# Optimization experiments

Hardware: AMD Instinct MI355X
Metric: run time of the kernel (lower is better)

## Reference

```python
import jax, jax.numpy as jnp
import numpy as np

NUM_HEADS = 16
ROPE_BASE = 10000.0


def _rope_cos_sin(seq_len, head_dim, dtype):
    inv_freq = 1.0 / (ROPE_BASE ** (jnp.arange(0, head_dim, 2, dtype=jnp.float32) / head_dim))
    t = jnp.arange(seq_len, dtype=jnp.float32)
    freqs = t[:, None] * inv_freq[None, :]          # [S, hd/2]
    emb = jnp.concatenate([freqs, freqs], axis=-1)  # [S, hd]
    return jnp.cos(emb).astype(dtype), jnp.sin(emb).astype(dtype)


def _rotate_half(x):
    x1, x2 = jnp.split(x, 2, axis=-1)
    return jnp.concatenate([-x2, x1], axis=-1)


def setup_inputs() -> dict:
    key = jax.random.key(0)
    ks = jax.random.split(key, 5)
    B, S, D = 2, 2048, 2048
    x = jax.random.normal(ks[0], (B, S, D), dtype=jnp.float32)
    Wq = jax.random.normal(ks[1], (D, D), dtype=jnp.float32) * (D ** -0.5)
    Wk = jax.random.normal(ks[2], (D, D), dtype=jnp.float32) * (D ** -0.5)
    Wv = jax.random.normal(ks[3], (D, D), dtype=jnp.float32) * (D ** -0.5)
    Wo = jax.random.normal(ks[4], (D, D), dtype=jnp.float32) * (D ** -0.5)
    return {"x": x, "Wq": Wq, "Wk": Wk, "Wv": Wv, "Wo": Wo}


def reference(x, Wq, Wk, Wv, Wo):
    B, S, D = x.shape
    H = NUM_HEADS
    hd = D // H
    scale = hd ** -0.5
    # Linear(bias=False): y = x @ W.T ; reshape to [B, H, S, hd]
    def proj(W):
        return jnp.einsum('bsd,ed->bse', x, W).reshape(B, S, H, hd).transpose(0, 2, 1, 3)
    q, k, v = proj(Wq), proj(Wk), proj(Wv)
    cos, sin = _rope_cos_sin(S, hd, x.dtype)  # [S, hd]
    cos = cos[None, None, :, :]
    sin = sin[None, None, :, :]
    q = q * cos + _rotate_half(q) * sin
    k = k * cos + _rotate_half(k) * sin
    scores = jnp.einsum('bhqd,bhkd->bhqk', q, k) * scale  # [B,H,S,S]
    causal = jnp.triu(jnp.ones((S, S), dtype=bool), k=1)
    scores = jnp.where(causal[None, None], jnp.finfo(scores.dtype).min, scores)
    attn = jax.nn.softmax(scores, axis=-1)
    out = jnp.einsum('bhqk,bhkd->bhqd', attn, v)  # [B,H,S,hd]
    out = out.transpose(0, 2, 1, 3).reshape(B, S, D)
    return jnp.einsum('bsd,ed->bse', out, Wo)
```

## Files before the change

kernel.cpp:

```cpp
#include <hip/hip_runtime.h>
#include <hip/hip_bf16.h>
#include <math.h>

typedef __bf16 bf16_t;
typedef __attribute__((ext_vector_type(8))) __bf16 bf16x8;
typedef __attribute__((ext_vector_type(4))) float f32x4;
typedef __attribute__((ext_vector_type(16))) float f32x16;

#define S_LEN 2048
#define DM    2048
#define NH    16
#define HD    128
#define MTOT  4096

__device__ inline float finz(float v) {
    return (v == v && fabsf(v) < 1e30f) ? v : 0.f;
}

__device__ inline void gload_lds16(const bf16_t* g, bf16_t* l) {
    __builtin_amdgcn_global_load_lds(
        (const __attribute__((address_space(1))) void*)g,
        (__attribute__((address_space(3))) void*)l, 16, 0, 0);
}

__device__ __forceinline__ int crow4(int g, int hi) {
    return (g & 3) + ((g >> 2) << 3) + (hi << 2);
}
__device__ __forceinline__ unsigned pk2(float x, float y) {
    union { bf16_t h; unsigned short u; } a, b;
    a.h = (bf16_t)x; b.h = (bf16_t)y;
    return (unsigned)a.u | ((unsigned)b.u << 16);
}
__device__ __forceinline__ bf16x8 pack4(unsigned w0, unsigned w1, unsigned w2, unsigned w3) {
    union { unsigned w[4]; bf16x8 v; } u;
    u.w[0] = w0; u.w[1] = w1; u.w[2] = w2; u.w[3] = w3;
    return u.v;
}

#define MFMA16(a, b, c) __builtin_amdgcn_mfma_f32_16x16x32_bf16(a, b, c, 0, 0, 0)
#define MFMA32(a, b, c) __builtin_amdgcn_mfma_f32_32x32x16_bf16(a, b, c, 0, 0, 0)

__global__ __launch_bounds__(256)
void dtype_probe(const unsigned short* __restrict__ p, unsigned int* __restrict__ flag)
{
    __shared__ int tot;
    if (threadIdx.x == 0) tot = 0;
    __syncthreads();
    int weird = 0;
    for (int i = threadIdx.x; i < 4096; i += 256) {
        unsigned short u = p[2*i];
        int e = (u >> 7) & 0xFF;
        if (e >= 0xC8 || (e != 0 && e <= 0x38)) weird++;
    }
    atomicAdd(&tot, weird);
    __syncthreads();
    if (threadIdx.x == 0) *flag = (tot > 512) ? 1u : 0u;
}

__global__ __launch_bounds__(256)
void convert_all(const void* __restrict__ x_raw,
                 const void* __restrict__ w0, const void* __restrict__ w1,
                 const void* __restrict__ w2, const void* __restrict__ w3,
                 bf16_t* __restrict__ xb, bf16_t* __restrict__ wb,
                 float2* __restrict__ rtab,
                 int mode, const unsigned int* __restrict__ flag)
{
    const int bid = blockIdx.x;
    if (bid >= 25088) return;
    if (bid >= 24576) {
        int i = (bid - 24576)*256 + threadIdx.x;
        int s = i >> 6, t64 = i & 63;
        float invf = exp2f(-(float)t64 * 0.20762050593046014f);
        float ang  = (float)s * invf;
        float sn, cs;
        sincosf(ang, &sn, &cs);
        rtab[i] = make_float2(cs, sn);
        return;
    }
    const bool f32 = (mode == 2) ? (*flag != 0) : (mode == 1);
    const void* src; bf16_t* dst; int i;
    if (bid < 8192) {
        src = x_raw; dst = xb; i = bid*1024 + threadIdx.x*4;
    } else {
        int w  = (bid - 8192) >> 12;
        int lb = (bid - 8192) & 4095;
        src = (w == 0) ? w0 : (w == 1) ? w1 : (w == 2) ? w2 : w3;
        dst = wb + (size_t)w * DM * DM;
        i = lb*1024 + threadIdx.x*4;
    }
    if (f32) {
        const float4 v = *(const float4*)((const float*)src + i);
        dst[i  ] = (bf16_t)v.x; dst[i+1] = (bf16_t)v.y;
        dst[i+2] = (bf16_t)v.z; dst[i+3] = (bf16_t)v.w;
    } else {
        *(uint2*)(dst + i) = *(const uint2*)((const bf16_t*)src + i);
    }
}

template<int MODE>
__global__ __launch_bounds__(256)
void gemm_bt(const bf16_t* __restrict__ A, const bf16_t* __restrict__ W,
             void* __restrict__ Cv, const float2* __restrict__ rtab)
{
    __shared__ __align__(16) bf16_t Sh[2*128*64];
    bf16_t* As = Sh;
    bf16_t* Ws = Sh + 128*64;

    const int t    = threadIdx.x;
    const int wv   = t >> 6;
    const int lane = t & 63;
    const int c16  = lane & 15;
    const int quad = lane >> 4;
    const int wm   = wv & 1;
    const int wn   = wv >> 1;
    const int mb   = blockIdx.x;
    const int nb   = blockIdx.y;
    const int c7   = c16 & 7;

    const int srow = lane >> 3;
    const int sphy = (lane & 7) ^ srow;
    const bf16_t* Ab = A + (size_t)(mb*128 + wv*32 + srow)*DM + sphy*8;
    const bf16_t* Wb = W + (size_t)(nb*128 + wv*32 + srow)*DM + sphy*8;

    f32x4 acc[4][4];
    #pragma unroll
    for (int i = 0; i < 4; ++i)
        #pragma unroll
        for (int j = 0; j < 4; ++j)
            acc[i][j] = (f32x4){0.f, 0.f, 0.f, 0.f};

    for (int kb = 0; kb < DM/64; ++kb) {
        __syncthreads();
        #pragma unroll
        for (int i = 0; i < 4; ++i) {
            gload_lds16(Ab + (size_t)kb*64 + (size_t)i*8*DM, As + (wv*32 + i*8)*64);
            gload_lds16(Wb + (size_t)kb*64 + (size_t)i*8*DM, Ws + (wv*32 + i*8)*64);
        }
        __syncthreads();

        #pragma unroll
        for (int kk = 0; kk < 2; ++kk) {
            const int ph = ((kk*4 + quad) ^ c7) * 8;
            bf16x8 af[4], bfr[4];
            #pragma unroll
            for (int mt = 0; mt < 4; ++mt)
                af[mt] = *(const bf16x8*)(As + (wm*64 + mt*16 + c16)*64 + ph);
            #pragma unroll
            for (int nt = 0; nt < 4; ++nt)
                bfr[nt] = *(const bf16x8*)(Ws + (nt*32 + wn*16 + c16)*64 + ph);
            #pragma unroll
            for (int mt = 0; mt < 4; ++mt)
                #pragma unroll
                for (int nt = 0; nt < 4; ++nt)
                    acc[mt][nt] = MFMA16(af[mt], bfr[nt], acc[mt][nt]);
        }
    }

    if (MODE == 4 && nb >= 32) {
        __syncthreads();
        #pragma unroll
        for (int mt = 0; mt < 4; ++mt) {
            #pragma unroll
            for (int r = 0; r < 4; ++r) {
                const int sl = wm*64 + mt*16 + quad*4 + r;
                #pragma unroll
                for (int nt = 0; nt < 4; ++nt) {
                    const int dl = nt*32 + wn*16 + c16;
                    Sh[dl*128 + (sl ^ ((dl & 15) << 3))] =
                        (bf16_t)finz(acc[mt][nt][r]);
                }
            }
        }
        __syncthreads();
        const int hh  = nb & 15;
        const int b   = (mb*128) >> 11;
        const int s0t = (mb*128) & (S_LEN - 1);
        bf16_t* VT = (bf16_t*)Cv + (size_t)2 * MTOT * DM;
        #pragma unroll
        for (int p = 0; p < 8; ++p) {
            int idx = p*256 + t;
            int dl  = idx >> 4;
            int s0  = (idx & 15) * 8;
            bf16x8 v = *(const bf16x8*)&Sh[dl*128 + (s0 ^ ((dl & 15) << 3))];
            *(bf16x8*)((bf16_t*)VT +
                ((size_t)(b*NH + hh)*HD + dl)*S_LEN + s0t + s0) = v;
        }
        return;
    }

    #pragma unroll
    for (int mt = 0; mt < 4; ++mt) {
        #pragma unroll
        for (int r = 0; r < 4; ++r) {
            const int m = mb*128 + wm*64 + mt*16 + quad*4 + r;
            if (MODE == 2) {
                bf16_t* C = (bf16_t*)Cv;
                size_t base = (size_t)m*DM + nb*128;
                #pragma unroll
                for (int nt = 0; nt < 4; ++nt)
                    C[base + nt*32 + wn*16 + c16] = (bf16_t)finz(acc[mt][nt][r]);
            } else if (MODE == 3) {
                float* C = (float*)Cv;
                size_t base = (size_t)m*DM + nb*128;
                #pragma unroll
                for (int nt = 0; nt < 4; ++nt)
                    C[base + nt*32 + wn*16 + c16] = finz(acc[mt][nt][r]);
            } else {
                const int g  = nb >> 4;
                const int hh = nb & 15;
                bf16_t* C = (bf16_t*)Cv + (size_t)g * MTOT * DM;
                const int b = m >> 11;
                const int s = m & (S_LEN - 1);
                size_t base = ((size_t)(b*NH + hh)*S_LEN + s)*HD;
                #pragma unroll
                for (int nt = 0; nt < 2; ++nt) {
                    int t64 = nt*32 + wn*16 + c16;
                    float2 cs2 = rtab[s*64 + t64];
                    float lo  = acc[mt][nt  ][r];
                    float hi2 = acc[mt][nt+2][r];
                    C[base + t64     ] = (bf16_t)finz(lo*cs2.x - hi2*cs2.y);
                    C[base + t64 + 64] = (bf16_t)finz(hi2*cs2.x + lo*cs2.y);
                }
            }
        }
    }
}

__global__ __launch_bounds__(512, 2)
void flash_attn(const bf16_t* __restrict__ Q, const bf16_t* __restrict__ K,
                const bf16_t* __restrict__ VT, bf16_t* __restrict__ O)
{
    __shared__ bf16_t Ks[64*128];
    __shared__ bf16_t Vs[128*64];
    __shared__ float  Ocmb[4][32*128];
    __shared__ float  lcmb[4][32];

    const int t    = threadIdx.x;
    const int wid  = t >> 6;
    const int lane = t & 63;
    const int qw   = wid & 3;
    const int kh   = wid >> 2;
    const int c32  = lane & 31;
    const int hi   = lane >> 5;
    const int bh   = blockIdx.x;
    const int ix   = blockIdx.y;

    const float scale = 0.08838834764831845f;
    const float SMAX  = 12.0f;

    bf16x8 onesf;
    #pragma unroll
    for (int j = 0; j < 8; ++j) onesf[j] = (bf16_t)1.0f;

    for (int pass = 0; pass < 2; ++pass) {
        const int Qt   = pass ? (15 - ix) : ix;
        const int qt0  = Qt * 128;
        const int qrow = qt0 + qw*32 + c32;
        const int qmin = qt0 + qw*32;

        bf16x8 qf[8];
        {
            const bf16_t* qp = Q + ((size_t)bh*S_LEN + qrow)*HD;
            #pragma unroll
            for (int s = 0; s < 8; ++s)
                qf[s] = *(const bf16x8*)(qp + s*16 + hi*8);
        }

        f32x16 oacc[4];
        f32x16 lacc;
        #pragma unroll
        for (int e = 0; e < 16; ++e) lacc[e] = 0.f;
        #pragma unroll
        for (int dt = 0; dt < 4; ++dt)
            #pragma unroll
            for (int e = 0; e < 16; ++e) oacc[dt][e] = 0.f;

        const int ktend = 2*Qt + 1;
        for (int kt = 0; kt <= ktend; ++kt) {
            __syncthreads();
            #pragma unroll
            for (int j = 0; j < 2; ++j) {
                int base = wid*8 + j*4;
                int rg   = base + (lane >> 4);
                int ph   = (lane & 15) ^ (rg & 7);
                gload_lds16(K + ((size_t)bh*S_LEN + kt*64 + rg)*HD + ph*8,
                            Ks + base*128);
            }
            #pragma unroll
            for (int j = 0; j < 2; ++j) {
                int base = wid*16 + j*8;
                int rg   = base + (lane >> 3);
                int ph   = (lane & 7) ^ (rg & 7);
                gload_lds16(VT + ((size_t)bh*HD + rg)*S_LEN + kt*64 + ph*8,
                            Vs + base*64);
            }
            __syncthreads();

            const int kbase = kt*64 + kh*32;
            if (kbase > qmin + 31) continue;

            f32x16 sacc;
            #pragma unroll
            for (int e = 0; e < 16; ++e) sacc[e] = 0.f;
            const int krow = kh*32 + c32;
            const int ksw  = krow & 7;
            __builtin_amdgcn_s_setprio(1);
            #pragma unroll
            for (int s = 0; s < 8; ++s) {
                bf16x8 kf = *(const bf16x8*)(Ks + krow*128 + (((s*2 + hi) ^ ksw) << 3));
                sacc = MFMA32(kf, qf[s], sacc);
            }
            __builtin_amdgcn_s_setprio(0);

            float p[16];
            if (kbase + 31 > qmin) {
                #pragma unroll
                for (int g = 0; g < 16; ++g) {
                    int kg = kbase + crow4(g, hi);
                    p[g] = (kg <= qrow) ? __expf(sacc[g]*scale - SMAX) : 0.f;
                }
            } else {
                #pragma unroll
                for (int g = 0; g < 16; ++g)
                    p[g] = __expf(sacc[g]*scale - SMAX);
            }

            unsigned a0 = pk2(p[0],  p[1]),  b0 = pk2(p[2],  p[3]);
            unsigned a1 = pk2(p[4],  p[5]),  b1 = pk2(p[6],  p[7]);
            unsigned a2 = pk2(p[8],  p[9]),  b2 = pk2(p[10], p[11]);
            unsigned a3 = pk2(p[12], p[13]), b3 = pk2(p[14], p[15]);
            asm volatile("v_permlane32_swap_b32 %0, %1" : "+v"(a0), "+v"(a1));
            asm volatile("v_permlane32_swap_b32 %0, %1" : "+v"(b0), "+v"(b1));
            asm volatile("v_permlane32_swap_b32 %0, %1" : "+v"(a2), "+v"(a3));
            asm volatile("v_permlane32_swap_b32 %0, %1" : "+v"(b2), "+v"(b3));
            bf16x8 pa0 = pack4(a0, b0, a1, b1);
            bf16x8 pa1 = pack4(a2, b2, a3, b3);

            const int ks0 = kh*2 + 0, ks1 = kh*2 + 1;
            __builtin_amdgcn_s_setprio(1);
            lacc = MFMA32(pa0, onesf, lacc);
            lacc = MFMA32(pa1, onesf, lacc);
            #pragma unroll
            for (int dt = 0; dt < 4; ++dt) {
                const int vrow = dt*32 + c32;
                const int vsw  = vrow & 7;
                bf16x8 vf0 = *(const bf16x8*)(Vs + vrow*64 + (((ks0*2 + hi) ^ vsw) << 3));
                oacc[dt] = MFMA32(pa0, vf0, oacc[dt]);
                bf16x8 vf1 = *(const bf16x8*)(Vs + vrow*64 + (((ks1*2 + hi) ^ vsw) << 3));
                oacc[dt] = MFMA32(pa1, vf1, oacc[dt]);
            }
            __builtin_amdgcn_s_setprio(0);
        }

        if (kh == 1) {
            #pragma unroll
            for (int g = 0; g < 16; ++g) {
                int ql = crow4(g, hi);
                #pragma unroll
                for (int dt = 0; dt < 4; ++dt)
                    Ocmb[qw][ql*128 + dt*32 + c32] = oacc[dt][g];
            }
            if (c32 == 0) {
                #pragma unroll
                for (int g = 0; g < 16; ++g)
                    lcmb[qw][crow4(g, hi)] = lacc[g];
            }
        }
        __syncthreads();
        if (kh == 0) {
            const int b = bh >> 4, h = bh & 15;
            #pragma unroll
            for (int g = 0; g < 16; ++g) {
                int ql = crow4(g, hi);
                int qg = qt0 + qw*32 + ql;
                float lt = lacc[g] + lcmb[qw][ql];
                float rl = 1.0f / fmaxf(lt, 1e-37f);
                #pragma unroll
                for (int dt = 0; dt < 4; ++dt) {
                    float v = oacc[dt][g] + Ocmb[qw][ql*128 + dt*32 + c32];
                    O[((size_t)(b*S_LEN + qg))*DM + h*HD + dt*32 + c32] =
                        (bf16_t)finz(v*rl);
                }
            }
        }
    }
}

extern "C" void kernel_launch(void* const* d_in, const int* in_sizes, int n_in,
                              void* d_out, int out_size, void* d_ws, size_t ws_size,
                              hipStream_t stream)
{
    const void* x_raw  = d_in[0];
    const void* Wq_raw = d_in[1];
    const void* Wk_raw = d_in[2];
    const void* Wv_raw = d_in[3];
    const void* Wo_raw = d_in[4];

    const int NX = MTOT*DM;
    const int NW = DM*DM;

    unsigned int* flag = (unsigned int*)d_ws;
    bf16_t* xb  = (bf16_t*)((char*)d_ws + 16);
    bf16_t* Wqb = xb  + NX;
    bf16_t* Wkb = Wqb + NW;
    bf16_t* Wvb = Wkb + NW;
    bf16_t* Wob = Wvb + NW;
    bf16_t* Qb  = Wob + NW;
    bf16_t* Kb  = Qb + NX;
    bf16_t* VTb = Kb + NX;
    bf16_t* Ob  = VTb + NX;
    float2* rtab = (float2*)(Ob + NX);

    bool out_is_f32 = true;
    {
        void* base = nullptr; size_t sz = 0;
        if (hipMemGetAddressRange((hipDeviceptr_t*)&base, &sz,
                                  (hipDeviceptr_t)d_out) == hipSuccess && sz != 0) {
            if (sz < (size_t)out_size * 3) out_is_f32 = false;
        }
    }

    int mode = 2;
    if (in_sizes && n_in >= 1) {
        if (in_sizes[0] == NX*4)      mode = 1;
        else if (in_sizes[0] == NX*2) mode = 0;
    }

    dim3 bb(256);
    if (mode == 2)
        hipLaunchKernelGGL(dtype_probe, dim3(1), bb, 0, stream,
                           (const unsigned short*)x_raw, flag);

    hipLaunchKernelGGL(convert_all, dim3(25088), bb, 0, stream,
                       x_raw, Wq_raw, Wk_raw, Wv_raw, Wo_raw,
                       xb, Wqb, rtab, mode, flag);

    hipLaunchKernelGGL((gemm_bt<4>), dim3(32, 48), bb, 0, stream, xb, Wqb,
                       (void*)Qb, rtab);
    hipLaunchKernelGGL(flash_attn, dim3(32, 8), dim3(512), 0, stream, Qb, Kb, VTb, Ob);
    if (out_is_f32)
        hipLaunchKernelGGL((gemm_bt<3>), dim3(32, 16), bb, 0, stream, Ob, Wob,
                           d_out, rtab);
    else
        hipLaunchKernelGGL((gemm_bt<2>), dim3(32, 16), bb, 0, stream, Ob, Wob,
                           d_out, rtab);
}
```

Before: 397.5 us.

## Fuse all stages into one persistent cooperative kernel with grid syncs

Replaces the five separate launches (dtype probe, conversion, QKV GEMM, flash attention, output GEMM) with one cooperative kernel of 256 blocks of 512 threads, separated by grid-wide barriers. Each block runs two 256-thread GEMM tile instances in its shared memory and grid-strides the conversion work. This is meant to remove launch overhead and inter-kernel gaps. In exchange the GEMM phases drop to one 512-thread block per CU with a fixed tile assignment, attention occupancy drops from launch_bounds(512,2) to (512,1), and grid.sync adds its own cost.

```diff
diff --git a/kernel.cpp b/kernel.cpp
--- a/kernel.cpp
+++ b/kernel.cpp
@@ -1,6 +1,9 @@
 #include <hip/hip_runtime.h>
+#include <hip/hip_cooperative_groups.h>
 #include <hip/hip_bf16.h>
 #include <math.h>
+
+namespace cg = cooperative_groups;
 
 typedef __bf16 bf16_t;
 typedef __attribute__((ext_vector_type(8))) __bf16 bf16x8;
@@ -40,81 +43,20 @@
 #define MFMA16(a, b, c) __builtin_amdgcn_mfma_f32_16x16x32_bf16(a, b, c, 0, 0, 0)
 #define MFMA32(a, b, c) __builtin_amdgcn_mfma_f32_32x32x16_bf16(a, b, c, 0, 0, 0)
 
-__global__ __launch_bounds__(256)
-void dtype_probe(const unsigned short* __restrict__ p, unsigned int* __restrict__ flag)
+__device__ __forceinline__ void gemm_tile(
+    bf16_t* __restrict__ Shm, const bf16_t* __restrict__ A,
+    const bf16_t* __restrict__ W, void* __restrict__ Cv,
+    const float2* __restrict__ rtab, int mb, int nb, int mode, int t)
 {
-    __shared__ int tot;
-    if (threadIdx.x == 0) tot = 0;
-    __syncthreads();
-    int weird = 0;
-    for (int i = threadIdx.x; i < 4096; i += 256) {
-        unsigned short u = p[2*i];
-        int e = (u >> 7) & 0xFF;
-        if (e >= 0xC8 || (e != 0 && e <= 0x38)) weird++;
-    }
-    atomicAdd(&tot, weird);
-    __syncthreads();
-    if (threadIdx.x == 0) *flag = (tot > 512) ? 1u : 0u;
-}
-
-__global__ __launch_bounds__(256)
-void convert_all(const void* __restrict__ x_raw,
-                 const void* __restrict__ w0, const void* __restrict__ w1,
-                 const void* __restrict__ w2, const void* __restrict__ w3,
-                 bf16_t* __restrict__ xb, bf16_t* __restrict__ wb,
-                 float2* __restrict__ rtab,
-                 int mode, const unsigned int* __restrict__ flag)
-{
-    const int bid = blockIdx.x;
-    if (bid >= 25088) return;
-    if (bid >= 24576) {
-        int i = (bid - 24576)*256 + threadIdx.x;
-        int s = i >> 6, t64 = i & 63;
-        float invf = exp2f(-(float)t64 * 0.20762050593046014f);
-        float ang  = (float)s * invf;
-        float sn, cs;
-        sincosf(ang, &sn, &cs);
-        rtab[i] = make_float2(cs, sn);
-        return;
-    }
-    const bool f32 = (mode == 2) ? (*flag != 0) : (mode == 1);
-    const void* src; bf16_t* dst; int i;
-    if (bid < 8192) {
-        src = x_raw; dst = xb; i = bid*1024 + threadIdx.x*4;
-    } else {
-        int w  = (bid - 8192) >> 12;
-        int lb = (bid - 8192) & 4095;
-        src = (w == 0) ? w0 : (w == 1) ? w1 : (w == 2) ? w2 : w3;
-        dst = wb + (size_t)w * DM * DM;
-        i = lb*1024 + threadIdx.x*4;
-    }
-    if (f32) {
-        const float4 v = *(const float4*)((const float*)src + i);
-        dst[i  ] = (bf16_t)v.x; dst[i+1] = (bf16_t)v.y;
-        dst[i+2] = (bf16_t)v.z; dst[i+3] = (bf16_t)v.w;
-    } else {
-        *(uint2*)(dst + i) = *(const uint2*)((const bf16_t*)src + i);
-    }
-}
-
-template<int MODE>
-__global__ __launch_bounds__(256)
-void gemm_bt(const bf16_t* __restrict__ A, const bf16_t* __restrict__ W,
-             void* __restrict__ Cv, const float2* __restrict__ rtab)
-{
-    __shared__ __align__(16) bf16_t Sh[2*128*64];
-    bf16_t* As = Sh;
-    bf16_t* Ws = Sh + 128*64;
-
-    const int t    = threadIdx.x;
+    bf16_t* As = Shm;
+    bf16_t* Ws = Shm + 128*64;
+
     const int wv   = t >> 6;
     const int lane = t & 63;
     const int c16  = lane & 15;
     const int quad = lane >> 4;
     const int wm   = wv & 1;
     const int wn   = wv >> 1;
-    const int mb   = blockIdx.x;
-    const int nb   = blockIdx.y;
     const int c7   = c16 & 7;
 
     const int srow = lane >> 3;
@@ -156,8 +98,9 @@
         }
     }
 
-    if (MODE == 4 && nb >= 32) {
-        __syncthreads();
+    const bool vpath = (mode == 4 && nb >= 32);
+    __syncthreads();
+    if (vpath) {
         #pragma unroll
         for (int mt = 0; mt < 4; ++mt) {
             #pragma unroll
@@ -166,12 +109,14 @@
                 #pragma unroll
                 for (int nt = 0; nt < 4; ++nt) {
                     const int dl = nt*32 + wn*16 + c16;
-                    Sh[dl*128 + (sl ^ ((dl & 15) << 3))] =
+                    Shm[dl*128 + (sl ^ ((dl & 15) << 3))] =
                         (bf16_t)finz(acc[mt][nt][r]);
                 }
             }
         }
-        __syncthreads();
+    }
+    __syncthreads();
+    if (vpath) {
         const int hh  = nb & 15;
         const int b   = (mb*128) >> 11;
         const int s0t = (mb*128) & (S_LEN - 1);
@@ -181,9 +126,8 @@
             int idx = p*256 + t;
             int dl  = idx >> 4;
             int s0  = (idx & 15) * 8;
-            bf16x8 v = *(const bf16x8*)&Sh[dl*128 + (s0 ^ ((dl & 15) << 3))];
-            *(bf16x8*)((bf16_t*)VT +
-                ((size_t)(b*NH + hh)*HD + dl)*S_LEN + s0t + s0) = v;
+            bf16x8 v = *(const bf16x8*)&Shm[dl*128 + (s0 ^ ((dl & 15) << 3))];
+            *(bf16x8*)(VT + ((size_t)(b*NH + hh)*HD + dl)*S_LEN + s0t + s0) = v;
         }
         return;
     }
@@ -193,13 +137,13 @@
         #pragma unroll
         for (int r = 0; r < 4; ++r) {
             const int m = mb*128 + wm*64 + mt*16 + quad*4 + r;
-            if (MODE == 2) {
+            if (mode == 2) {
                 bf16_t* C = (bf16_t*)Cv;
                 size_t base = (size_t)m*DM + nb*128;
                 #pragma unroll
                 for (int nt = 0; nt < 4; ++nt)
                     C[base + nt*32 + wn*16 + c16] = (bf16_t)finz(acc[mt][nt][r]);
-            } else if (MODE == 3) {
+            } else if (mode == 3) {
                 float* C = (float*)Cv;
                 size_t base = (size_t)m*DM + nb*128;
                 #pragma unroll
@@ -226,163 +170,276 @@
     }
 }
 
-__global__ __launch_bounds__(512, 2)
-void flash_attn(const bf16_t* __restrict__ Q, const bf16_t* __restrict__ K,
-                const bf16_t* __restrict__ VT, bf16_t* __restrict__ O)
+__global__ __launch_bounds__(512, 1)
+void mha_fused(const void* __restrict__ x_raw,
+               const void* __restrict__ w0, const void* __restrict__ w1,
+               const void* __restrict__ w2, const void* __restrict__ w3,
+               bf16_t* __restrict__ xb, bf16_t* __restrict__ wb,
+               bf16_t* __restrict__ Qb, bf16_t* __restrict__ Ob,
+               void* __restrict__ Cout, float2* __restrict__ rtab,
+               int mode, int outf)
 {
-    __shared__ bf16_t Ks[64*128];
-    __shared__ bf16_t Vs[128*64];
-    __shared__ float  Ocmb[4][32*128];
-    __shared__ float  lcmb[4][32];
-
-    const int t    = threadIdx.x;
-    const int wid  = t >> 6;
-    const int lane = t & 63;
-    const int qw   = wid & 3;
-    const int kh   = wid >> 2;
-    const int c32  = lane & 31;
-    const int hi   = lane >> 5;
-    const int bh   = blockIdx.x;
-    const int ix   = blockIdx.y;
-
-    const float scale = 0.08838834764831845f;
-    const float SMAX  = 12.0f;
-
-    bf16x8 onesf;
-    #pragma unroll
-    for (int j = 0; j < 8; ++j) onesf[j] = (bf16_t)1.0f;
-
-    for (int pass = 0; pass < 2; ++pass) {
-        const int Qt   = pass ? (15 - ix) : ix;
-        const int qt0  = Qt * 128;
-        const int qrow = qt0 + qw*32 + c32;
-        const int qmin = qt0 + qw*32;
-
-        bf16x8 qf[8];
+    __shared__ __align__(16) unsigned char ShRaw[98816];
+    cg::grid_group grid = cg::this_grid();
+
+    const int bid = blockIdx.x;
+    const int t   = threadIdx.x;
+    const int NXE = MTOT*DM;
+    const int NWE = DM*DM;
+
+    {
+        bool f32in;
+        if (mode == 2) {
+            int* tot = (int*)ShRaw;
+            if (t == 0) *tot = 0;
+            __syncthreads();
+            int weird = 0;
+            const unsigned short* p = (const unsigned short*)x_raw;
+            for (int i = t; i < 4096; i += 512) {
+                unsigned short u = p[2*i];
+                int e = (u >> 7) & 0xFF;
+                if (e >= 0xC8 || (e != 0 && e <= 0x38)) weird++;
+            }
+            atomicAdd(tot, weird);
+            __syncthreads();
+            f32in = (*tot > 512);
+            __syncthreads();
+        } else {
+            f32in = (mode == 1);
+        }
+
+        const int gtid = bid*512 + t;
+        const int GSTR = 256*512;
+        if (f32in) {
+            for (int i = gtid; i < NXE/4; i += GSTR) {
+                float4 v = ((const float4*)x_raw)[i];
+                union { bf16_t h[4]; uint2 u; } o;
+                o.h[0] = (bf16_t)v.x; o.h[1] = (bf16_t)v.y;
+                o.h[2] = (bf16_t)v.z; o.h[3] = (bf16_t)v.w;
+                ((uint2*)xb)[i] = o.u;
+            }
+            const void* wsrc[4] = {w0, w1, w2, w3};
+            #pragma unroll
+            for (int w = 0; w < 4; ++w) {
+                const float4* ws = (const float4*)wsrc[w];
+                uint2* wd = (uint2*)(wb + (size_t)w*NWE);
+                for (int i = gtid; i < NWE/4; i += GSTR) {
+                    float4 v = ws[i];
+                    union { bf16_t h[4]; uint2 u; } o;
+                    o.h[0] = (bf16_t)v.x; o.h[1] = (bf16_t)v.y;
+                    o.h[2] = (bf16_t)v.z; o.h[3] = (bf16_t)v.w;
+                    wd[i] = o.u;
+                }
+            }
+        } else {
+            for (int i = gtid; i < NXE/4; i += GSTR)
+                ((uint2*)xb)[i] = ((const uint2*)x_raw)[i];
+            const void* wsrc[4] = {w0, w1, w2, w3};
+            #pragma unroll
+            for (int w = 0; w < 4; ++w) {
+                const uint2* ws = (const uint2*)wsrc[w];
+                uint2* wd = (uint2*)(wb + (size_t)w*NWE);
+                for (int i = gtid; i < NWE/4; i += GSTR)
+                    wd[i] = ws[i];
+            }
+        }
         {
-            const bf16_t* qp = Q + ((size_t)bh*S_LEN + qrow)*HD;
-            #pragma unroll
-            for (int s = 0; s < 8; ++s)
-                qf[s] = *(const bf16x8*)(qp + s*16 + hi*8);
-        }
-
-        f32x16 oacc[4];
-        f32x16 lacc;
-        #pragma unroll
-        for (int e = 0; e < 16; ++e) lacc[e] = 0.f;
-        #pragma unroll
-        for (int dt = 0; dt < 4; ++dt)
-            #pragma unroll
-            for (int e = 0; e < 16; ++e) oacc[dt][e] = 0.f;
-
-        const int ktend = 2*Qt + 1;
-        for (int kt = 0; kt <= ktend; ++kt) {
+            int i = gtid;
+            int s = i >> 6, t64 = i & 63;
+            float invf = exp2f(-(float)t64 * 0.20762050593046014f);
+            float ang  = (float)s * invf;
+            float sn, cs;
+            sincosf(ang, &sn, &cs);
+            rtab[i] = make_float2(cs, sn);
+        }
+    }
+    __threadfence();
+    grid.sync();
+
+    {
+        const int inst = t >> 8;
+        const int t4   = t & 255;
+        bf16_t* Shm = (bf16_t*)(ShRaw + inst*32768);
+        #pragma unroll
+        for (int j2 = 0; j2 < 3; ++j2) {
+            int tile = bid + 256*(j2*2 + inst);
+            gemm_tile(Shm, xb, wb, (void*)Qb, rtab, tile & 31, tile >> 5, 4, t4);
+        }
+    }
+    __threadfence();
+    grid.sync();
+
+    {
+        bf16_t* Ks   = (bf16_t*)ShRaw;
+        bf16_t* Vs   = (bf16_t*)(ShRaw + 16384);
+        float*  Ocmb = (float*)(ShRaw + 32768);
+        float*  lcmb = (float*)(ShRaw + 98304);
+        const bf16_t* Q  = Qb;
+        const bf16_t* K  = Qb + (size_t)NXE;
+        const bf16_t* VT = Qb + (size_t)2*NXE;
+        bf16_t* O = Ob;
+
+        const int wid  = t >> 6;
+        const int lane = t & 63;
+        const int qw   = wid & 3;
+        const int kh   = wid >> 2;
+        const int c32  = lane & 31;
+        const int hi   = lane >> 5;
+        const int bh   = bid & 31;
+        const int ix   = bid >> 5;
+
+        const float scale = 0.08838834764831845f;
+        const float SMAX  = 12.0f;
+
+        bf16x8 onesf;
+        #pragma unroll
+        for (int j = 0; j < 8; ++j) onesf[j] = (bf16_t)1.0f;
+
+        for (int pass = 0; pass < 2; ++pass) {
+            const int Qt   = pass ? (15 - ix) : ix;
+            const int qt0  = Qt * 128;
+            const int qrow = qt0 + qw*32 + c32;
+            const int qmin = qt0 + qw*32;
+
+            bf16x8 qf[8];
+            {
+                const bf16_t* qp = Q + ((size_t)bh*S_LEN + qrow)*HD;
+                #pragma unroll
+                for (int s = 0; s < 8; ++s)
+                    qf[s] = *(const bf16x8*)(qp + s*16 + hi*8);
+            }
+
+            f32x16 oacc[4];
+            f32x16 lacc;
+            #pragma unroll
+            for (int e = 0; e < 16; ++e) lacc[e] = 0.f;
+            #pragma unroll
+            for (int dt = 0; dt < 4; ++dt)
+                #pragma unroll
+                for (int e = 0; e < 16; ++e) oacc[dt][e] = 0.f;
+
+            const int ktend = 2*Qt + 1;
+            for (int kt = 0; kt <= ktend; ++kt) {
+                __syncthreads();
+                #pragma unroll
+                for (int j = 0; j < 2; ++j) {
+                    int base = wid*8 + j*4;
+                    int rg   = base + (lane >> 4);
+                    int ph   = (lane & 15) ^ (rg & 7);
+                    gload_lds16(K + ((size_t)bh*S_LEN + kt*64 + rg)*HD + ph*8,
+                                Ks + base*128);
+                }
+                #pragma unroll
+                for (int j = 0; j < 2; ++j) {
+                    int base = wid*16 + j*8;
+                    int rg   = base + (lane >> 3);
+                    int ph   = (lane & 7) ^ (rg & 7);
+                    gload_lds16(VT + ((size_t)bh*HD + rg)*S_LEN + kt*64 + ph*8,
+                                Vs + base*64);
+                }
+                __syncthreads();
+
+                const int kbase = kt*64 + kh*32;
+                if (kbase > qmin + 31) continue;
+
+                f32x16 sacc;
+                #pragma unroll
+                for (int e = 0; e < 16; ++e) sacc[e] = 0.f;
+                const int krow = kh*32 + c32;
+                const int ksw  = krow & 7;
+                __builtin_amdgcn_s_setprio(1);
+                #pragma unroll
+                for (int s = 0; s < 8; ++s) {
+                    bf16x8 kf = *(const bf16x8*)(Ks + krow*128 + (((s*2 + hi) ^ ksw) << 3));
+                    sacc = MFMA32(kf, qf[s], sacc);
+                }
+                __builtin_amdgcn_s_setprio(0);
+
+                float p[16];
+                if (kbase + 31 > qmin) {
+                    #pragma unroll
+                    for (int g = 0; g < 16; ++g) {
+                        int kg = kbase + crow4(g, hi);
+                        p[g] = (kg <= qrow) ? __expf(sacc[g]*scale - SMAX) : 0.f;
+                    }
+                } else {
+                    #pragma unroll
+                    for (int g = 0; g < 16; ++g)
+                        p[g] = __expf(sacc[g]*scale - SMAX);
+                }
+
+                unsigned a0 = pk2(p[0],  p[1]),  b0 = pk2(p[2],  p[3]);
+                unsigned a1 = pk2(p[4],  p[5]),  b1 = pk2(p[6],  p[7]);
+                unsigned a2 = pk2(p[8],  p[9]),  b2 = pk2(p[10], p[11]);
+                unsigned a3 = pk2(p[12], p[13]), b3 = pk2(p[14], p[15]);
+                asm volatile("v_permlane32_swap_b32 %0, %1" : "+v"(a0), "+v"(a1));
+                asm volatile("v_permlane32_swap_b32 %0, %1" : "+v"(b0), "+v"(b1));
+                asm volatile("v_permlane32_swap_b32 %0, %1" : "+v"(a2), "+v"(a3));
+                asm volatile("v_permlane32_swap_b32 %0, %1" : "+v"(b2), "+v"(b3));
+                bf16x8 pa0 = pack4(a0, b0, a1, b1);
+                bf16x8 pa1 = pack4(a2, b2, a3, b3);
+
+                const int ks0 = kh*2 + 0, ks1 = kh*2 + 1;
+                __builtin_amdgcn_s_setprio(1);
+                lacc = MFMA32(pa0, onesf, lacc);
+                lacc = MFMA32(pa1, onesf, lacc);
+                #pragma unroll
+                for (int dt = 0; dt < 4; ++dt) {
+                    const int vrow = dt*32 + c32;
+                    const int vsw  = vrow & 7;
+                    bf16x8 vf0 = *(const bf16x8*)(Vs + vrow*64 + (((ks0*2 + hi) ^ vsw) << 3));
+                    oacc[dt] = MFMA32(pa0, vf0, oacc[dt]);
+                    bf16x8 vf1 = *(const bf16x8*)(Vs + vrow*64 + (((ks1*2 + hi) ^ vsw) << 3));
+                    oacc[dt] = MFMA32(pa1, vf1, oacc[dt]);
+                }
+                __builtin_amdgcn_s_setprio(0);
+            }
+
+            if (kh == 1) {
+                #pragma unroll
+                for (int g = 0; g < 16; ++g) {
+                    int ql = crow4(g, hi);
+                    #pragma unroll
+                    for (int dt = 0; dt < 4; ++dt)
+                        Ocmb[qw*4096 + ql*128 + dt*32 + c32] = oacc[dt][g];
+                }
+                if (c32 == 0) {
+                    #pragma unroll
+                    for (int g = 0; g < 16; ++g)
+                        lcmb[qw*32 + crow4(g, hi)] = lacc[g];
+                }
+            }
             __syncthreads();
-            #pragma unroll
-            for (int j = 0; j < 2; ++j) {
-                int base = wid*8 + j*4;
-                int rg   = base + (lane >> 4);
-                int ph   = (lane & 15) ^ (rg & 7);
-                gload_lds16(K + ((size_t)bh*S_LEN + kt*64 + rg)*HD + ph*8,
-                            Ks + base*128);
-            }
-            #pragma unroll
-            for (int j = 0; j < 2; ++j) {
-                int base = wid*16 + j*8;
-                int rg   = base + (lane >> 3);
-                int ph   = (lane & 7) ^ (rg & 7);
-                gload_lds16(VT + ((size_t)bh*HD + rg)*S_LEN + kt*64 + ph*8,
-                            Vs + base*64);
+            if (kh == 0) {
+                const int b = bh >> 4, h = bh & 15;
+                #pragma unroll
+                for (int g = 0; g < 16; ++g) {
+                    int ql = crow4(g, hi);
+                    int qg = qt0 + qw*32 + ql;
+                    float lt = lacc[g] + lcmb[qw*32 + ql];
+                    float rl = 1.0f / fmaxf(lt, 1e-37f);
+                    #pragma unroll
+                    for (int dt = 0; dt < 4; ++dt) {
+                        float v = oacc[dt][g] + Ocmb[qw*4096 + ql*128 + dt*32 + c32];
+                        O[((size_t)(b*S_LEN + qg))*DM + h*HD + dt*32 + c32] =
+                            (bf16_t)finz(v*rl);
+                    }
+                }
             }
             __syncthreads();
-
-            const int kbase = kt*64 + kh*32;
-            if (kbase > qmin + 31) continue;
-
-            f32x16 sacc;
-            #pragma unroll
-            for (int e = 0; e < 16; ++e) sacc[e] = 0.f;
-            const int krow = kh*32 + c32;
-            const int ksw  = krow & 7;
-            __builtin_amdgcn_s_setprio(1);
-            #pragma unroll
-            for (int s = 0; s < 8; ++s) {
-                bf16x8 kf = *(const bf16x8*)(Ks + krow*128 + (((s*2 + hi) ^ ksw) << 3));
-                sacc = MFMA32(kf, qf[s], sacc);
-            }
-            __builtin_amdgcn_s_setprio(0);
-
-            float p[16];
-            if (kbase + 31 > qmin) {
-                #pragma unroll
-                for (int g = 0; g < 16; ++g) {
-                    int kg = kbase + crow4(g, hi);
-                    p[g] = (kg <= qrow) ? __expf(sacc[g]*scale - SMAX) : 0.f;
-                }
-            } else {
-                #pragma unroll
-                for (int g = 0; g < 16; ++g)
-                    p[g] = __expf(sacc[g]*scale - SMAX);
-            }
-
-            unsigned a0 = pk2(p[0],  p[1]),  b0 = pk2(p[2],  p[3]);
-            unsigned a1 = pk2(p[4],  p[5]),  b1 = pk2(p[6],  p[7]);
-            unsigned a2 = pk2(p[8],  p[9]),  b2 = pk2(p[10], p[11]);
-            unsigned a3 = pk2(p[12], p[13]), b3 = pk2(p[14], p[15]);
-            asm volatile("v_permlane32_swap_b32 %0, %1" : "+v"(a0), "+v"(a1));
-            asm volatile("v_permlane32_swap_b32 %0, %1" : "+v"(b0), "+v"(b1));
-            asm volatile("v_permlane32_swap_b32 %0, %1" : "+v"(a2), "+v"(a3));
-            asm volatile("v_permlane32_swap_b32 %0, %1" : "+v"(b2), "+v"(b3));
-            bf16x8 pa0 = pack4(a0, b0, a1, b1);
-            bf16x8 pa1 = pack4(a2, b2, a3, b3);
-
-            const int ks0 = kh*2 + 0, ks1 = kh*2 + 1;
-            __builtin_amdgcn_s_setprio(1);
-            lacc = MFMA32(pa0, onesf, lacc);
-            lacc = MFMA32(pa1, onesf, lacc);
-            #pragma unroll
-            for (int dt = 0; dt < 4; ++dt) {
-                const int vrow = dt*32 + c32;
-                const int vsw  = vrow & 7;
-                bf16x8 vf0 = *(const bf16x8*)(Vs + vrow*64 + (((ks0*2 + hi) ^ vsw) << 3));
-                oacc[dt] = MFMA32(pa0, vf0, oacc[dt]);
-                bf16x8 vf1 = *(const bf16x8*)(Vs + vrow*64 + (((ks1*2 + hi) ^ vsw) << 3));
-                oacc[dt] = MFMA32(pa1, vf1, oacc[dt]);
-            }
-            __builtin_amdgcn_s_setprio(0);
-        }
-
-        if (kh == 1) {
-            #pragma unroll
-            for (int g = 0; g < 16; ++g) {
-                int ql = crow4(g, hi);
-                #pragma unroll
-                for (int dt = 0; dt < 4; ++dt)
-                    Ocmb[qw][ql*128 + dt*32 + c32] = oacc[dt][g];
-            }
-            if (c32 == 0) {
-                #pragma unroll
-                for (int g = 0; g < 16; ++g)
-                    lcmb[qw][crow4(g, hi)] = lacc[g];
-            }
-        }
-        __syncthreads();
-        if (kh == 0) {
-            const int b = bh >> 4, h = bh & 15;
-            #pragma unroll
-            for (int g = 0; g < 16; ++g) {
-                int ql = crow4(g, hi);
-                int qg = qt0 + qw*32 + ql;
-                float lt = lacc[g] + lcmb[qw][ql];
-                float rl = 1.0f / fmaxf(lt, 1e-37f);
-                #pragma unroll
-                for (int dt = 0; dt < 4; ++dt) {
-                    float v = oacc[dt][g] + Ocmb[qw][ql*128 + dt*32 + c32];
-                    O[((size_t)(b*S_LEN + qg))*DM + h*HD + dt*32 + c32] =
-                        (bf16_t)finz(v*rl);
-                }
-            }
-        }
+        }
+    }
+    __threadfence();
+    grid.sync();
+
+    {
+        const int inst = t >> 8;
+        const int t4   = t & 255;
+        bf16_t* Shm = (bf16_t*)(ShRaw + inst*32768);
+        bf16_t* Wob = wb + (size_t)3*NWE;
+        int tile = bid + 256*inst;
+        gemm_tile(Shm, Ob, Wob, Cout, rtab, tile & 31, tile >> 5,
+                  outf ? 3 : 2, t4);
     }
 }
 
@@ -399,16 +456,10 @@
     const int NX = MTOT*DM;
     const int NW = DM*DM;
 
-    unsigned int* flag = (unsigned int*)d_ws;
     bf16_t* xb  = (bf16_t*)((char*)d_ws + 16);
     bf16_t* Wqb = xb  + NX;
-    bf16_t* Wkb = Wqb + NW;
-    bf16_t* Wvb = Wkb + NW;
-    bf16_t* Wob = Wvb + NW;
-    bf16_t* Qb  = Wob + NW;
-    bf16_t* Kb  = Qb + NX;
-    bf16_t* VTb = Kb + NX;
-    bf16_t* Ob  = VTb + NX;
+    bf16_t* Qb  = Wqb + 4*(size_t)NW;
+    bf16_t* Ob  = Qb + 3*(size_t)NX;
     float2* rtab = (float2*)(Ob + NX);
 
     bool out_is_f32 = true;
@@ -425,23 +476,13 @@
         if (in_sizes[0] == NX*4)      mode = 1;
         else if (in_sizes[0] == NX*2) mode = 0;
     }
-
-    dim3 bb(256);
-    if (mode == 2)
-        hipLaunchKernelGGL(dtype_probe, dim3(1), bb, 0, stream,
-                           (const unsigned short*)x_raw, flag);
-
-    hipLaunchKernelGGL(convert_all, dim3(25088), bb, 0, stream,
-                       x_raw, Wq_raw, Wk_raw, Wv_raw, Wo_raw,
-                       xb, Wqb, rtab, mode, flag);
-
-    hipLaunchKernelGGL((gemm_bt<4>), dim3(32, 48), bb, 0, stream, xb, Wqb,
-                       (void*)Qb, rtab);
-    hipLaunchKernelGGL(flash_attn, dim3(32, 8), dim3(512), 0, stream, Qb, Kb, VTb, Ob);
-    if (out_is_f32)
-        hipLaunchKernelGGL((gemm_bt<3>), dim3(32, 16), bb, 0, stream, Ob, Wob,
-                           d_out, rtab);
-    else
-        hipLaunchKernelGGL((gemm_bt<2>), dim3(32, 16), bb, 0, stream, Ob, Wob,
-                           d_out, rtab);
-}
+    int outf = out_is_f32 ? 1 : 0;
+
+    void* args[] = {
+        (void*)&x_raw, (void*)&Wq_raw, (void*)&Wk_raw, (void*)&Wv_raw,
+        (void*)&Wo_raw, (void*)&xb, (void*)&Wqb, (void*)&Qb, (void*)&Ob,
+        (void*)&d_out, (void*)&rtab, (void*)&mode, (void*)&outf
+    };
+    hipLaunchCooperativeKernel((const void*)mha_fused, dim3(256), dim3(512),
+                               args, 0, stream);
+}
```

Result: slower. 773.6 us (+94.6%).
